# Performance work log

Measured on AMD Instinct MI355X. Metric: run time of the kernel, lower is better.

Reference implementation:

```python
import jax, jax.numpy as jnp
import numpy as np

R = 16      # box filter radius (init kwarg)
EPS = 1e-4  # regularization (init kwarg)


def _diff_x(src, r):
    c = jnp.cumsum(src, axis=-2)
    left = c[..., r:2 * r + 1, :]
    middle = c[..., 2 * r + 1:, :] - c[..., :-2 * r - 1, :]
    right = c[..., -1:, :] - c[..., -2 * r - 1:-r - 1, :]
    return jnp.concatenate([left, middle, right], axis=-2)


def _diff_y(src, r):
    c = jnp.cumsum(src, axis=-1)
    left = c[..., r:2 * r + 1]
    middle = c[..., 2 * r + 1:] - c[..., :-2 * r - 1]
    right = c[..., -1:] - c[..., -2 * r - 1:-r - 1]
    return jnp.concatenate([left, middle, right], axis=-1)


def boxfilter2d(src, radius):
    return _diff_y(_diff_x(src, radius), radius)


def guidedfilter2d_color(guide, src, radius, eps):
    # guide: (B,3,H,W), src: (B,C,H,W)
    g_r, g_g, g_b = guide[:, 0:1], guide[:, 1:2], guide[:, 2:3]
    ones = jnp.ones_like(g_r)
    N = boxfilter2d(ones, radius)                       # (B,1,H,W)
    mean_I = boxfilter2d(guide, radius) / N             # (B,3,H,W)
    mI_r, mI_g, mI_b = mean_I[:, 0:1], mean_I[:, 1:2], mean_I[:, 2:3]
    mean_p = boxfilter2d(src, radius) / N               # (B,C,H,W)
    mean_Ip_r = boxfilter2d(g_r * src, radius) / N
    mean_Ip_g = boxfilter2d(g_g * src, radius) / N
    mean_Ip_b = boxfilter2d(g_b * src, radius) / N
    cov_Ip_r = mean_Ip_r - mI_r * mean_p
    cov_Ip_g = mean_Ip_g - mI_g * mean_p
    cov_Ip_b = mean_Ip_b - mI_b * mean_p
    v_rr = boxfilter2d(g_r * g_r, radius) / N - mI_r * mI_r + eps
    v_rg = boxfilter2d(g_r * g_g, radius) / N - mI_r * mI_g
    v_rb = boxfilter2d(g_r * g_b, radius) / N - mI_r * mI_b
    v_gg = boxfilter2d(g_g * g_g, radius) / N - mI_g * mI_g + eps
    v_gb = boxfilter2d(g_g * g_b, radius) / N - mI_g * mI_b
    v_bb = boxfilter2d(g_b * g_b, radius) / N - mI_b * mI_b + eps
    det = (v_rr * v_gg * v_bb + v_rg * v_gb * v_rb + v_rb * v_rg * v_gb
           - v_rb * v_gg * v_rb - v_rg * v_rg * v_bb - v_rr * v_gb * v_gb)
    i_rr = (v_gg * v_bb - v_gb * v_gb) / det
    i_rg = -(v_rg * v_bb - v_rb * v_gb) / det
    i_rb = (v_rg * v_gb - v_rb * v_gg) / det
    i_gg = (v_rr * v_bb - v_rb * v_rb) / det
    i_gb = -(v_rr * v_gb - v_rb * v_rg) / det
    i_bb = (v_rr * v_gg - v_rg * v_rg) / det
    # inv_sigma: (B,3,3,H,W) per-pixel inverse covariance
    inv_sigma = jnp.stack([
        jnp.stack([i_rr, i_rg, i_rb], axis=1),
        jnp.stack([i_rg, i_gg, i_gb], axis=1),
        jnp.stack([i_rb, i_gb, i_bb], axis=1)], axis=1)[..., 0, :, :]
    cov_Ip = jnp.stack([cov_Ip_r, cov_Ip_g, cov_Ip_b], axis=1)  # (B,3,C,H,W)
    a = jnp.einsum('bichw,bijhw->bjchw', cov_Ip, inv_sigma)     # (B,3,C,H,W)
    b = mean_p - a[:, 0] * mI_r - a[:, 1] * mI_g - a[:, 2] * mI_b
    mean_a = boxfilter2d(a, radius) / N[:, None]                # (B,3,C,H,W)
    mean_b = boxfilter2d(b, radius) / N
    q = jnp.einsum('bichw,bihw->bchw', mean_a, guide) + mean_b
    return q


def setup_inputs() -> dict:
    key = jax.random.key(0)
    k1, k2 = jax.random.split(key)
    guide = jax.random.uniform(k1, (1, 3, 2048, 2048), dtype=jnp.float32)
    src = jax.random.uniform(k2, (1, 3, 2048, 2048), dtype=jnp.float32)
    return {"guide": guide, "src": src}


def reference(guide, src):
    return guidedfilter2d_color(guide, src, R, EPS)
```

## Files before the change

kernel.cpp:

```cpp
#include <hip/hip_runtime.h>
#include <cstdio>
#include <cstdint>

#define HH 2048
#define WWI 2048
#define RAD 16
#define EPSF 1e-4f
#define BRA 16
#define BRB 32
#define W_OUT 94

typedef _Float16 h16;
constexpr size_t PLN = (size_t)HH * WWI;
constexpr int ROWB = WWI * 4;

__device__ __forceinline__ int cnt1d(int p, int n) {
    int lo = p - RAD; if (lo < 0) lo = 0;
    int hi = p + RAD; if (hi > n - 1) hi = n - 1;
    return hi - lo + 1;
}

__device__ __forceinline__ float ldf(const float* __restrict__ p, int boff) {
    return *reinterpret_cast<const float*>(reinterpret_cast<const char*>(p) + boff);
}
__device__ __forceinline__ float2 ldf2(const float* __restrict__ p, int boff) {
    return *reinterpret_cast<const float2*>(reinterpret_cast<const char*>(p) + boff);
}
__device__ __forceinline__ uint32_t ldu(const uint32_t* __restrict__ p, int boff) {
    return *reinterpret_cast<const uint32_t*>(reinterpret_cast<const char*>(p) + boff);
}
__device__ __forceinline__ void stu2(uint32_t* __restrict__ p, int boff, uint2 v) {
    *reinterpret_cast<uint2*>(reinterpret_cast<char*>(p) + boff) = v;
}
__device__ __forceinline__ void stf(float* __restrict__ p, int boff, float v) {
    *reinterpret_cast<float*>(reinterpret_cast<char*>(p) + boff) = v;
}
__device__ __forceinline__ uint32_t pk(float a, float b) {
    union { h16 h[2]; uint32_t u; } t;
    t.h[0] = (h16)a; t.h[1] = (h16)b; return t.u;
}
__device__ __forceinline__ float2 upk(uint32_t u) {
    union { uint32_t u; h16 h[2]; } t; t.u = u;
    return make_float2((float)t.h[0], (float)t.h[1]);
}

template<int CTRL, int RM>
__device__ __forceinline__ float dpp_add(float x) {
    int t = __builtin_amdgcn_update_dpp(0, __builtin_bit_cast(int, x), CTRL, RM, 0xf, false);
    return x + __builtin_bit_cast(float, t);
}
__device__ __forceinline__ float wscan(float x) {
    x = dpp_add<0x111, 0xf>(x);
    x = dpp_add<0x112, 0xf>(x);
    x = dpp_add<0x114, 0xf>(x);
    x = dpp_add<0x118, 0xf>(x);
    x = dpp_add<0x142, 0xa>(x);
    x = dpp_add<0x143, 0xc>(x);
    return x;
}
__device__ __forceinline__ float bperm(int byteaddr, float v) {
    return __builtin_bit_cast(float,
        __builtin_amdgcn_ds_bpermute(byteaddr, __builtin_bit_cast(int, v)));
}

template<bool ADD>
__device__ __forceinline__ void prod21(float v0, float v1, float v2,
                                       float v3, float v4, float v5, float S[21]) {
    float p[21];
    p[0] = v0; p[1] = v1; p[2] = v2; p[3] = v3; p[4] = v4; p[5] = v5;
    p[6] = v0 * v3; p[7] = v0 * v4; p[8] = v0 * v5;
    p[9] = v1 * v3; p[10] = v1 * v4; p[11] = v1 * v5;
    p[12] = v2 * v3; p[13] = v2 * v4; p[14] = v2 * v5;
    p[15] = v0 * v0; p[16] = v0 * v1; p[17] = v0 * v2;
    p[18] = v1 * v1; p[19] = v1 * v2; p[20] = v2 * v2;
#pragma unroll
    for (int c = 0; c < 21; ++c) { if constexpr (ADD) S[c] += p[c]; else S[c] -= p[c]; }
}

template<bool ADD>
__device__ __forceinline__ void acc12(const uint32_t* __restrict__ a0, const uint32_t* __restrict__ a1,
                                      const uint32_t* __restrict__ a2, const uint32_t* __restrict__ a3,
                                      const uint32_t* __restrict__ a4, const uint32_t* __restrict__ a5,
                                      int boff, bool ok, float S[12]) {
    if (!ok) return;
    const uint32_t u0 = ldu(a0, boff), u1 = ldu(a1, boff), u2 = ldu(a2, boff);
    const uint32_t u3 = ldu(a3, boff), u4 = ldu(a4, boff), u5 = ldu(a5, boff);
    const float2 f0 = upk(u0), f1 = upk(u1), f2 = upk(u2);
    const float2 f3 = upk(u3), f4 = upk(u4), f5 = upk(u5);
    if constexpr (ADD) {
        S[0] += f0.x; S[1] += f0.y; S[2] += f1.x; S[3] += f1.y;
        S[4] += f2.x; S[5] += f2.y; S[6] += f3.x; S[7] += f3.y;
        S[8] += f4.x; S[9] += f4.y; S[10] += f5.x; S[11] += f5.y;
    } else {
        S[0] -= f0.x; S[1] -= f0.y; S[2] -= f1.x; S[3] -= f1.y;
        S[4] -= f2.x; S[5] -= f2.y; S[6] -= f3.x; S[7] -= f3.y;
        S[8] -= f4.x; S[9] -= f4.y; S[10] -= f5.x; S[11] -= f5.y;
    }
}

__device__ __forceinline__ void solve_ab(const float S[21], float rN, float o[12]) {
    const float m0 = S[0] * rN, m1 = S[1] * rN, m2 = S[2] * rN;
    const float p0 = S[3] * rN, p1 = S[4] * rN, p2 = S[5] * rN;
    const float c00 = S[6] * rN - m0 * p0;
    const float c01 = S[7] * rN - m0 * p1;
    const float c02 = S[8] * rN - m0 * p2;
    const float c10 = S[9] * rN - m1 * p0;
    const float c11 = S[10] * rN - m1 * p1;
    const float c12 = S[11] * rN - m1 * p2;
    const float c20 = S[12] * rN - m2 * p0;
    const float c21 = S[13] * rN - m2 * p1;
    const float c22 = S[14] * rN - m2 * p2;
    const float vrr = S[15] * rN - m0 * m0 + EPSF;
    const float vrg = S[16] * rN - m0 * m1;
    const float vrb = S[17] * rN - m0 * m2;
    const float vgg = S[18] * rN - m1 * m1 + EPSF;
    const float vgb = S[19] * rN - m1 * m2;
    const float vbb = S[20] * rN - m2 * m2 + EPSF;
    const float det = vrr * vgg * vbb + vrg * vgb * vrb + vrb * vrg * vgb
                    - vrb * vgg * vrb - vrg * vrg * vbb - vrr * vgb * vgb;
    const float id = __builtin_amdgcn_rcpf(det);
    const float irr =  (vgg * vbb - vgb * vgb) * id;
    const float irg = -(vrg * vbb - vrb * vgb) * id;
    const float irb =  (vrg * vgb - vrb * vgg) * id;
    const float igg =  (vrr * vbb - vrb * vrb) * id;
    const float igb = -(vrr * vgb - vrb * vrg) * id;
    const float ibb =  (vrr * vgg - vrg * vrg) * id;
    const float a00 = c00 * irr + c10 * irg + c20 * irb;
    const float a01 = c01 * irr + c11 * irg + c21 * irb;
    const float a02 = c02 * irr + c12 * irg + c22 * irb;
    const float a10 = c00 * irg + c10 * igg + c20 * igb;
    const float a11 = c01 * irg + c11 * igg + c21 * igb;
    const float a12 = c02 * irg + c12 * igg + c22 * igb;
    const float a20 = c00 * irb + c10 * igb + c20 * ibb;
    const float a21 = c01 * irb + c11 * igb + c21 * ibb;
    const float a22 = c02 * irb + c12 * igb + c22 * ibb;
    o[0] = a00; o[1] = a01; o[2] = a02;
    o[3] = a10; o[4] = a11; o[5] = a12;
    o[6] = a20; o[7] = a21; o[8] = a22;
    o[9]  = p0 - a00 * m0 - a10 * m1 - a20 * m2;
    o[10] = p1 - a01 * m0 - a11 * m1 - a21 * m2;
    o[11] = p2 - a02 * m0 - a12 * m1 - a22 * m2;
}

#define LOAD6F(P, bo) { P[0] = ldf2(g0, bo); P[1] = ldf2(g1, bo); P[2] = ldf2(g2, bo); \
                        P[3] = ldf2(s0, bo); P[4] = ldf2(s1, bo); P[5] = ldf2(s2, bo); }
#define LOAD6U(P, bo) { P[0] = ldu(a0, bo); P[1] = ldu(a1, bo); P[2] = ldu(a2, bo); \
                        P[3] = ldu(a3, bo); P[4] = ldu(a4, bo); P[5] = ldu(a5, bo); }

__global__ __launch_bounds__(128, 3) void kA(const float* __restrict__ g,
                                             const float* __restrict__ s,
                                             uint32_t* __restrict__ ab) {
    const int lid = blockIdx.y * 11 + blockIdx.x;
    const int swz = (lid & 7) * 176 + (lid >> 3);
    const int bx  = swz % 11;
    const int by  = swz / 11;

    const int lane = threadIdx.x & 63;
    const int wv   = bx * 2 + (threadIdx.x >> 6);
    const int W0   = wv * W_OUT;
    const int X0   = W0 - 18;
    const int col0 = X0 + 2 * lane;
    const bool okc = (unsigned)col0 < (unsigned)WWI;
    const int colb = (okc ? col0 : 0) * 4;
    const int r0   = by * BRA;
    const int aP17 = ((lane + 17) & 63) * 4;
    const int aP1  = ((lane + 1) & 63) * 4;
    const int j0   = W0 + 2 * lane;
    const bool outl = (lane <= 46) && (j0 < WWI);

    const float* g0 = g;         const float* g1 = g + PLN;   const float* g2 = g + 2 * PLN;
    const float* s0 = s;         const float* s1 = s + PLN;   const float* s2 = s + 2 * PLN;
    uint32_t* a0 = ab;           uint32_t* a1 = ab + PLN;     uint32_t* a2 = ab + 2 * PLN;
    uint32_t* a3 = ab + 3 * PLN; uint32_t* a4 = ab + 4 * PLN; uint32_t* a5 = ab + 5 * PLN;

    float S0[21], S1[21];
#pragma unroll
    for (int c = 0; c < 21; ++c) { S0[c] = 0.f; S1[c] = 0.f; }
    {
        int lo = r0 - RAD; if (lo < 0) lo = 0;
        int hi = r0 + RAD; if (hi > HH - 1) hi = HH - 1;
        int r = lo;
        if (okc) {
            int boff = lo * ROWB + col0 * 4;
            for (; r + 3 <= hi; r += 4) {
                float2 R0[6], R1[6], R2[6], R3[6];
                LOAD6F(R0, boff);
                LOAD6F(R1, boff + ROWB);
                LOAD6F(R2, boff + 2 * ROWB);
                LOAD6F(R3, boff + 3 * ROWB);
                prod21<true>(R0[0].x, R0[1].x, R0[2].x, R0[3].x, R0[4].x, R0[5].x, S0);
                prod21<true>(R0[0].y, R0[1].y, R0[2].y, R0[3].y, R0[4].y, R0[5].y, S1);
                prod21<true>(R1[0].x, R1[1].x, R1[2].x, R1[3].x, R1[4].x, R1[5].x, S0);
                prod21<true>(R1[0].y, R1[1].y, R1[2].y, R1[3].y, R1[4].y, R1[5].y, S1);
                prod21<true>(R2[0].x, R2[1].x, R2[2].x, R2[3].x, R2[4].x, R2[5].x, S0);
                prod21<true>(R2[0].y, R2[1].y, R2[2].y, R2[3].y, R2[4].y, R2[5].y, S1);
                prod21<true>(R3[0].x, R3[1].x, R3[2].x, R3[3].x, R3[4].x, R3[5].x, S0);
                prod21<true>(R3[0].y, R3[1].y, R3[2].y, R3[3].y, R3[4].y, R3[5].y, S1);
                boff += 4 * ROWB;
            }
            for (; r <= hi; ++r) {
                float2 R0[6];
                LOAD6F(R0, boff);
                prod21<true>(R0[0].x, R0[1].x, R0[2].x, R0[3].x, R0[4].x, R0[5].x, S0);
                prod21<true>(R0[0].y, R0[1].y, R0[2].y, R0[3].y, R0[4].y, R0[5].y, S1);
                boff += ROWB;
            }
        }
    }
    const float cx0 = (float)cnt1d(j0, WWI);
    const float cx1 = (float)cnt1d(j0 + 1, WWI);
    int oOff = r0 * ROWB + j0 * 4;
    for (int ii = 0; ii < BRA; ++ii) {
        const int i = r0 + ii;
        float2 PA[6], PB[6];
        const bool doAdv = (ii + 1 < BRA);
        if (doAdv) {
            const int boA = min(i + RAD + 1, HH - 1) * ROWB + colb;
            const int boB = max(i - RAD, 0) * ROWB + colb;
            LOAD6F(PA, boA);
            LOAD6F(PB, boB);
        }
        float H0[21], H1[21];
#pragma unroll
        for (int c = 0; c < 21; ++c) {
            const float PP  = wscan(S0[c] + S1[c]);
            const float ppa = bperm(aP17, PP);
            const float s1b = bperm(aP17, S1[c]);
            const float s0b = bperm(aP1,  S0[c]);
            const float D = ppa - PP;
            H0[c] = D - s1b;
            H1[c] = D - s0b;
        }
        if (doAdv) {
#pragma unroll
            for (int k = 0; k < 6; ++k) {
                PA[k].x = okc ? PA[k].x : 0.f; PA[k].y = okc ? PA[k].y : 0.f;
                PB[k].x = okc ? PB[k].x : 0.f; PB[k].y = okc ? PB[k].y : 0.f;
            }
            if (i + RAD + 1 < HH) {
                prod21<true>(PA[0].x, PA[1].x, PA[2].x, PA[3].x, PA[4].x, PA[5].x, S0);
                prod21<true>(PA[0].y, PA[1].y, PA[2].y, PA[3].y, PA[4].y, PA[5].y, S1);
            }
            if (i - RAD >= 0) {
                prod21<false>(PB[0].x, PB[1].x, PB[2].x, PB[3].x, PB[4].x, PB[5].x, S0);
                prod21<false>(PB[0].y, PB[1].y, PB[2].y, PB[3].y, PB[4].y, PB[5].y, S1);
            }
        }
        const float cy = (float)cnt1d(i, HH);
        float o0[12], o1[12];
        solve_ab(H0, __builtin_amdgcn_rcpf(cx0 * cy), o0);
        solve_ab(H1, __builtin_amdgcn_rcpf(cx1 * cy), o1);
        if (outl) {
            stu2(a0, oOff, make_uint2(pk(o0[0],  o0[1]),  pk(o1[0],  o1[1])));
            stu2(a1, oOff, make_uint2(pk(o0[2],  o0[3]),  pk(o1[2],  o1[3])));
            stu2(a2, oOff, make_uint2(pk(o0[4],  o0[5]),  pk(o1[4],  o1[5])));
            stu2(a3, oOff, make_uint2(pk(o0[6],  o0[7]),  pk(o1[6],  o1[7])));
            stu2(a4, oOff, make_uint2(pk(o0[8],  o0[9]),  pk(o1[8],  o1[9])));
            stu2(a5, oOff, make_uint2(pk(o0[10], o0[11]), pk(o1[10], o1[11])));
        }
        oOff += ROWB;
    }
}

__global__ __launch_bounds__(256) void kB(const uint32_t* __restrict__ ab,
                                          const float* __restrict__ g,
                                          float* __restrict__ outp) {
    const int lid = blockIdx.y * 16 + blockIdx.x;
    const int swz = (lid & 7) * 128 + (lid >> 3);
    const int bx  = swz & 15;
    const int by  = swz >> 4;

    const int lane = threadIdx.x & 63;
    const int wv   = bx * 4 + (threadIdx.x >> 6);
    const int x0   = wv * 32;
    const int col  = x0 - RAD + lane;
    const bool okc = (unsigned)col < (unsigned)WWI;
    const int colb = (okc ? col : 0) * 4;
    const int r0   = by * BRB;
    const int addrA = ((lane + 16) & 63) * 4;
    const int addrB = (lane >= 17 ? lane - 17 : 0) * 4;
    const bool subok = lane >= 17;
    const bool outl  = (lane >= 16) && (lane < 48);

    const uint32_t* a0 = ab;           const uint32_t* a1 = ab + PLN;     const uint32_t* a2 = ab + 2 * PLN;
    const uint32_t* a3 = ab + 3 * PLN; const uint32_t* a4 = ab + 4 * PLN; const uint32_t* a5 = ab + 5 * PLN;
    const float* g0 = g;  const float* g1 = g + PLN;  const float* g2 = g + 2 * PLN;
    float* o0 = outp;     float* o1 = outp + PLN;     float* o2 = outp + 2 * PLN;

    float S[12];
#pragma unroll
    for (int c = 0; c < 12; ++c) S[c] = 0.f;
    {
        int lo = r0 - RAD; if (lo < 0) lo = 0;
        int hi = r0 + RAD; if (hi > HH - 1) hi = HH - 1;
        int boff = lo * ROWB + col * 4;
        for (int r = lo; r <= hi; ++r) {
            acc12<true>(a0, a1, a2, a3, a4, a5, boff, okc, S);
            boff += ROWB;
        }
    }
    const float cx = (float)cnt1d(col, WWI);
    int oOff = r0 * ROWB + col * 4;

    uint32_t UA[6], UB[6], UA2[6], UB2[6];
    {
        const int boA = min(r0 + RAD + 1, HH - 1) * ROWB + colb;
        const int boB = max(r0 - RAD, 0) * ROWB + colb;
        LOAD6U(UA, boA);
        LOAD6U(UB, boB);
    }
    for (int ii = 0; ii < BRB; ++ii) {
        const int i = r0 + ii;
        if (ii + 1 < BRB) {
            const int boA = min(i + RAD + 2, HH - 1) * ROWB + colb;
            const int boB = max(i + 1 - RAD, 0) * ROWB + colb;
            LOAD6U(UA2, boA);
            LOAD6U(UB2, boB);
        }
        float H[12];
#pragma unroll
        for (int c = 0; c < 12; ++c) {
            const float sc = wscan(S[c]);
            const float hv = bperm(addrA, sc);
            const float lv = bperm(addrB, sc);
            H[c] = hv - (subok ? lv : 0.f);
        }
        if (ii + 1 < BRB) {
#pragma unroll
            for (int k = 0; k < 6; ++k) {
                UA[k] = okc ? UA[k] : 0u;
                UB[k] = okc ? UB[k] : 0u;
            }
            if (i + RAD + 1 < HH) {
#pragma unroll
                for (int k = 0; k < 6; ++k) {
                    const float2 f = upk(UA[k]);
                    S[2 * k] += f.x; S[2 * k + 1] += f.y;
                }
            }
            if (i - RAD >= 0) {
#pragma unroll
                for (int k = 0; k < 6; ++k) {
                    const float2 f = upk(UB[k]);
                    S[2 * k] -= f.x; S[2 * k + 1] -= f.y;
                }
            }
        }
        if (outl) {
            const float rN = __builtin_amdgcn_rcpf(cx * (float)cnt1d(i, HH));
            const float gg0 = ldf(g0, oOff), gg1 = ldf(g1, oOff), gg2 = ldf(g2, oOff);
            stf(o0, oOff, (H[0] * gg0 + H[3] * gg1 + H[6] * gg2 + H[9])  * rN);
            stf(o1, oOff, (H[1] * gg0 + H[4] * gg1 + H[7] * gg2 + H[10]) * rN);
            stf(o2, oOff, (H[2] * gg0 + H[5] * gg1 + H[8] * gg2 + H[11]) * rN);
        }
#pragma unroll
        for (int k = 0; k < 6; ++k) { UA[k] = UA2[k]; UB[k] = UB2[k]; }
        oOff += ROWB;
    }
}

extern "C" void kernel_launch(void* const* d_in, const int* in_sizes, int n_in,
                              void* d_out, int out_size, void* d_ws, size_t ws_size,
                              hipStream_t stream) {
    const float* g = (const float*)d_in[0];
    const float* s = (const float*)d_in[1];
    float* outp = (float*)d_out;
    uint32_t* ab = (uint32_t*)d_ws;

    const size_t need = 6 * PLN * sizeof(uint32_t);
    if (ws_size < need)
        fprintf(stderr, "[gf] WARNING ws_size=%zu < need=%zu\n", ws_size, need);

    kA<<<dim3(11, HH / BRA, 1), dim3(128, 1, 1), 0, stream>>>(g, s, ab);
    kB<<<dim3(WWI / 128, HH / BRB, 1), dim3(256, 1, 1), 0, stream>>>(ab, g, outp);
}
```

Baseline: 176.2 us.

## Split kA's 21 moment channels across two waves with LDS exchange

Before, each wave of kA handled one column strip and kept all 21 moment sums for two columns. Now the two waves of a block share a strip: each accumulates and horizontally scans about half of the moments (11 per wave, one overlapping), then swaps the partial horizontal sums through shared memory so each wave can solve the 3x3 system for one of the two columns. The grid doubles to 22 blocks across. This cuts register pressure and per-wave scan work, but adds a __syncthreads per row, LDS traffic, duplicate global loads of the same inputs by both waves, and narrower 4-byte stores.

```diff
diff --git a/kernel.cpp b/kernel.cpp
--- a/kernel.cpp
+++ b/kernel.cpp
@@ -29,8 +29,8 @@
 __device__ __forceinline__ uint32_t ldu(const uint32_t* __restrict__ p, int boff) {
     return *reinterpret_cast<const uint32_t*>(reinterpret_cast<const char*>(p) + boff);
 }
-__device__ __forceinline__ void stu2(uint32_t* __restrict__ p, int boff, uint2 v) {
-    *reinterpret_cast<uint2*>(reinterpret_cast<char*>(p) + boff) = v;
+__device__ __forceinline__ void stu(uint32_t* __restrict__ p, int boff, uint32_t v) {
+    *reinterpret_cast<uint32_t*>(reinterpret_cast<char*>(p) + boff) = v;
 }
 __device__ __forceinline__ void stf(float* __restrict__ p, int boff, float v) {
     *reinterpret_cast<float*>(reinterpret_cast<char*>(p) + boff) = v;
@@ -63,18 +63,25 @@
         __builtin_amdgcn_ds_bpermute(byteaddr, __builtin_bit_cast(int, v)));
 }
 
+template<int CB, bool ADD>
+__device__ __forceinline__ void prodR(const float v[6], float S[11]) {
+    static constexpr int IA[21] = {0,1,2,3,4,5, 0,0,0, 1,1,1, 2,2,2, 0,0,0, 1,1, 2};
+    static constexpr int IB[21] = {-1,-1,-1,-1,-1,-1, 3,4,5, 3,4,5, 3,4,5, 0,1,2, 1,2, 2};
+#pragma unroll
+    for (int k = 0; k < 11; ++k) {
+        float p = v[IA[CB + k]];
+        if (IB[CB + k] >= 0) p *= v[IB[CB + k]];
+        if constexpr (ADD) S[k] += p; else S[k] -= p;
+    }
+}
+
 template<bool ADD>
-__device__ __forceinline__ void prod21(float v0, float v1, float v2,
-                                       float v3, float v4, float v5, float S[21]) {
-    float p[21];
-    p[0] = v0; p[1] = v1; p[2] = v2; p[3] = v3; p[4] = v4; p[5] = v5;
-    p[6] = v0 * v3; p[7] = v0 * v4; p[8] = v0 * v5;
-    p[9] = v1 * v3; p[10] = v1 * v4; p[11] = v1 * v5;
-    p[12] = v2 * v3; p[13] = v2 * v4; p[14] = v2 * v5;
-    p[15] = v0 * v0; p[16] = v0 * v1; p[17] = v0 * v2;
-    p[18] = v1 * v1; p[19] = v1 * v2; p[20] = v2 * v2;
-#pragma unroll
-    for (int c = 0; c < 21; ++c) { if constexpr (ADD) S[c] += p[c]; else S[c] -= p[c]; }
+__device__ __forceinline__ void accRowRole(int wid, const float2 R[6],
+                                           float S0[11], float S1[11]) {
+    const float vx[6] = {R[0].x, R[1].x, R[2].x, R[3].x, R[4].x, R[5].x};
+    const float vy[6] = {R[0].y, R[1].y, R[2].y, R[3].y, R[4].y, R[5].y};
+    if (wid == 0) { prodR<0,  ADD>(vx, S0); prodR<0,  ADD>(vy, S1); }
+    else          { prodR<10, ADD>(vx, S0); prodR<10, ADD>(vy, S1); }
 }
 
 template<bool ADD>
@@ -150,14 +157,15 @@
 __global__ __launch_bounds__(128, 3) void kA(const float* __restrict__ g,
                                              const float* __restrict__ s,
                                              uint32_t* __restrict__ ab) {
-    const int lid = blockIdx.y * 11 + blockIdx.x;
-    const int swz = (lid & 7) * 176 + (lid >> 3);
-    const int bx  = swz % 11;
-    const int by  = swz / 11;
+    __shared__ float xh[2][20][64];
+    const int lid = blockIdx.y * 22 + blockIdx.x;
+    const int swz = (lid & 7) * 352 + (lid >> 3);
+    const int bx  = swz % 22;
+    const int by  = swz / 22;
 
     const int lane = threadIdx.x & 63;
-    const int wv   = bx * 2 + (threadIdx.x >> 6);
-    const int W0   = wv * W_OUT;
+    const int wid  = threadIdx.x >> 6;
+    const int W0   = bx * W_OUT;
     const int X0   = W0 - 18;
     const int col0 = X0 + 2 * lane;
     const bool okc = (unsigned)col0 < (unsigned)WWI;
@@ -165,17 +173,17 @@
     const int r0   = by * BRA;
     const int aP17 = ((lane + 17) & 63) * 4;
     const int aP1  = ((lane + 1) & 63) * 4;
-    const int j0   = W0 + 2 * lane;
-    const bool outl = (lane <= 46) && (j0 < WWI);
+    const int jc   = W0 + 2 * lane + wid;
+    const bool outl = (lane <= 46) && (jc < WWI);
 
     const float* g0 = g;         const float* g1 = g + PLN;   const float* g2 = g + 2 * PLN;
     const float* s0 = s;         const float* s1 = s + PLN;   const float* s2 = s + 2 * PLN;
     uint32_t* a0 = ab;           uint32_t* a1 = ab + PLN;     uint32_t* a2 = ab + 2 * PLN;
     uint32_t* a3 = ab + 3 * PLN; uint32_t* a4 = ab + 4 * PLN; uint32_t* a5 = ab + 5 * PLN;
 
-    float S0[21], S1[21];
-#pragma unroll
-    for (int c = 0; c < 21; ++c) { S0[c] = 0.f; S1[c] = 0.f; }
+    float S0[11], S1[11];
+#pragma unroll
+    for (int k = 0; k < 11; ++k) { S0[k] = 0.f; S1[k] = 0.f; }
     {
         int lo = r0 - RAD; if (lo < 0) lo = 0;
         int hi = r0 + RAD; if (hi > HH - 1) hi = HH - 1;
@@ -188,30 +196,25 @@
                 LOAD6F(R1, boff + ROWB);
                 LOAD6F(R2, boff + 2 * ROWB);
                 LOAD6F(R3, boff + 3 * ROWB);
-                prod21<true>(R0[0].x, R0[1].x, R0[2].x, R0[3].x, R0[4].x, R0[5].x, S0);
-                prod21<true>(R0[0].y, R0[1].y, R0[2].y, R0[3].y, R0[4].y, R0[5].y, S1);
-                prod21<true>(R1[0].x, R1[1].x, R1[2].x, R1[3].x, R1[4].x, R1[5].x, S0);
-                prod21<true>(R1[0].y, R1[1].y, R1[2].y, R1[3].y, R1[4].y, R1[5].y, S1);
-                prod21<true>(R2[0].x, R2[1].x, R2[2].x, R2[3].x, R2[4].x, R2[5].x, S0);
-                prod21<true>(R2[0].y, R2[1].y, R2[2].y, R2[3].y, R2[4].y, R2[5].y, S1);
-                prod21<true>(R3[0].x, R3[1].x, R3[2].x, R3[3].x, R3[4].x, R3[5].x, S0);
-                prod21<true>(R3[0].y, R3[1].y, R3[2].y, R3[3].y, R3[4].y, R3[5].y, S1);
+                accRowRole<true>(wid, R0, S0, S1);
+                accRowRole<true>(wid, R1, S0, S1);
+                accRowRole<true>(wid, R2, S0, S1);
+                accRowRole<true>(wid, R3, S0, S1);
                 boff += 4 * ROWB;
             }
             for (; r <= hi; ++r) {
                 float2 R0[6];
                 LOAD6F(R0, boff);
-                prod21<true>(R0[0].x, R0[1].x, R0[2].x, R0[3].x, R0[4].x, R0[5].x, S0);
-                prod21<true>(R0[0].y, R0[1].y, R0[2].y, R0[3].y, R0[4].y, R0[5].y, S1);
+                accRowRole<true>(wid, R0, S0, S1);
                 boff += ROWB;
             }
         }
     }
-    const float cx0 = (float)cnt1d(j0, WWI);
-    const float cx1 = (float)cnt1d(j0 + 1, WWI);
-    int oOff = r0 * ROWB + j0 * 4;
+    const float cxc = (float)cnt1d(jc, WWI);
+    int oOff = r0 * ROWB + jc * 4;
     for (int ii = 0; ii < BRA; ++ii) {
         const int i = r0 + ii;
+        const int buf = ii & 1;
         float2 PA[6], PB[6];
         const bool doAdv = (ii + 1 < BRA);
         if (doAdv) {
@@ -220,16 +223,36 @@
             LOAD6F(PA, boA);
             LOAD6F(PB, boB);
         }
-        float H0[21], H1[21];
-#pragma unroll
-        for (int c = 0; c < 21; ++c) {
-            const float PP  = wscan(S0[c] + S1[c]);
+        float myH0[11], myH1[11];
+#pragma unroll
+        for (int k = 0; k < 11; ++k) {
+            const float PP  = wscan(S0[k] + S1[k]);
             const float ppa = bperm(aP17, PP);
-            const float s1b = bperm(aP17, S1[c]);
-            const float s0b = bperm(aP1,  S0[c]);
+            const float s1b = bperm(aP17, S1[k]);
+            const float s0b = bperm(aP1,  S0[k]);
             const float D = ppa - PP;
-            H0[c] = D - s1b;
-            H1[c] = D - s0b;
+            myH0[k] = D - s1b;
+            myH1[k] = D - s0b;
+        }
+        if (wid == 0) {
+#pragma unroll
+            for (int k = 0; k < 10; ++k) xh[buf][k][lane] = myH1[k];
+        } else {
+#pragma unroll
+            for (int k = 1; k < 11; ++k) xh[buf][9 + k][lane] = myH0[k];
+        }
+        __syncthreads();
+        float H[21];
+        if (wid == 0) {
+#pragma unroll
+            for (int k = 0; k < 11; ++k) H[k] = myH0[k];
+#pragma unroll
+            for (int c = 11; c < 21; ++c) H[c] = xh[buf][c - 1][lane];
+        } else {
+#pragma unroll
+            for (int c = 0; c < 10; ++c) H[c] = xh[buf][c][lane];
+#pragma unroll
+            for (int k = 0; k < 11; ++k) H[10 + k] = myH1[k];
         }
         if (doAdv) {
 #pragma unroll
@@ -237,26 +260,19 @@
                 PA[k].x = okc ? PA[k].x : 0.f; PA[k].y = okc ? PA[k].y : 0.f;
                 PB[k].x = okc ? PB[k].x : 0.f; PB[k].y = okc ? PB[k].y : 0.f;
             }
-            if (i + RAD + 1 < HH) {
-                prod21<true>(PA[0].x, PA[1].x, PA[2].x, PA[3].x, PA[4].x, PA[5].x, S0);
-                prod21<true>(PA[0].y, PA[1].y, PA[2].y, PA[3].y, PA[4].y, PA[5].y, S1);
-            }
-            if (i - RAD >= 0) {
-                prod21<false>(PB[0].x, PB[1].x, PB[2].x, PB[3].x, PB[4].x, PB[5].x, S0);
-                prod21<false>(PB[0].y, PB[1].y, PB[2].y, PB[3].y, PB[4].y, PB[5].y, S1);
-            }
+            if (i + RAD + 1 < HH) accRowRole<true >(wid, PA, S0, S1);
+            if (i - RAD >= 0)     accRowRole<false>(wid, PB, S0, S1);
         }
         const float cy = (float)cnt1d(i, HH);
-        float o0[12], o1[12];
-        solve_ab(H0, __builtin_amdgcn_rcpf(cx0 * cy), o0);
-        solve_ab(H1, __builtin_amdgcn_rcpf(cx1 * cy), o1);
+        float o[12];
+        solve_ab(H, __builtin_amdgcn_rcpf(cxc * cy), o);
         if (outl) {
-            stu2(a0, oOff, make_uint2(pk(o0[0],  o0[1]),  pk(o1[0],  o1[1])));
-            stu2(a1, oOff, make_uint2(pk(o0[2],  o0[3]),  pk(o1[2],  o1[3])));
-            stu2(a2, oOff, make_uint2(pk(o0[4],  o0[5]),  pk(o1[4],  o1[5])));
-            stu2(a3, oOff, make_uint2(pk(o0[6],  o0[7]),  pk(o1[6],  o1[7])));
-            stu2(a4, oOff, make_uint2(pk(o0[8],  o0[9]),  pk(o1[8],  o1[9])));
-            stu2(a5, oOff, make_uint2(pk(o0[10], o0[11]), pk(o1[10], o1[11])));
+            stu(a0, oOff, pk(o[0],  o[1]));
+            stu(a1, oOff, pk(o[2],  o[3]));
+            stu(a2, oOff, pk(o[4],  o[5]));
+            stu(a3, oOff, pk(o[6],  o[7]));
+            stu(a4, oOff, pk(o[8],  o[9]));
+            stu(a5, oOff, pk(o[10], o[11]));
         }
         oOff += ROWB;
     }
@@ -371,6 +387,6 @@
     if (ws_size < need)
         fprintf(stderr, "[gf] WARNING ws_size=%zu < need=%zu\n", ws_size, need);
 
-    kA<<<dim3(11, HH / BRA, 1), dim3(128, 1, 1), 0, stream>>>(g, s, ab);
+    kA<<<dim3(22, HH / BRA, 1), dim3(128, 1, 1), 0, stream>>>(g, s, ab);
     kB<<<dim3(WWI / 128, HH / BRB, 1), dim3(256, 1, 1), 0, stream>>>(ab, g, outp);
 }
```

New measurement: 198.7 us. 12.8% more time.
